# Kernel tuning notes

Hardware: AMD Instinct MI355X
Metric: run time of the kernel (lower is better)

Reference implementation:

```python
import jax, jax.numpy as jnp
import numpy as np

MASK_OUT_VALUE = -10000.0


def setup_inputs() -> dict:
    key = jax.random.key(0)
    k1, k2, k3 = jax.random.split(key, 3)
    B, H, S, D = 2, 16, 2048, 64
    query = jax.random.normal(k1, (B, H, S, D), dtype=jnp.float32)
    key_t = jax.random.normal(k2, (B, H, S, D), dtype=jnp.float32)
    value = jax.random.normal(k3, (B, H, S, D), dtype=jnp.float32)
    # causal mask: (1, 1, S, S), True where attention is allowed
    mask = jnp.tril(jnp.ones((S, S), dtype=bool))[None, None, :, :]
    return {"query": query, "key": key_t, "value": value, "mask": mask}


def reference(query, key, value, mask):
    # scores: (B, H, S, S)
    scale = 1.0 / jnp.sqrt(jnp.asarray(query.shape[-1], query.dtype))
    attn_scores = jnp.einsum("bhqd,bhkd->bhqk", query, key) * scale
    attn_scores = jnp.where(mask, attn_scores,
                            jnp.asarray(MASK_OUT_VALUE, attn_scores.dtype))
    attn_weights = jax.nn.softmax(attn_scores, axis=-1)
    # dropout is identity (p=0 / eval mode)
    attn_output = jnp.einsum("bhqk,bhkd->bhqd", attn_weights, value)
    return attn_output
```

## Files before the change

### kernel.cpp

```cpp
#include <hip/hip_runtime.h>
#include <math.h>


#define S_LEN   2048
#define D_HEAD  64
#define SCALE_L2E 0.18033688011112042f
#define FIXM    8.0f

using bf16x8 = __attribute__((ext_vector_type(8))) short;
using f32x4  = __attribute__((ext_vector_type(4))) float;

__device__ __forceinline__ unsigned int rnd_bf(float f) {
  return __float_as_uint(f) + 0x8000u;
}
__device__ __forceinline__ unsigned short f2bf(float f) {
  return (unsigned short)(rnd_bf(f) >> 16);
}

__device__ __forceinline__ void gl_lds16(const unsigned short* g, unsigned short* l) {
  __builtin_amdgcn_global_load_lds(
      (const __attribute__((address_space(1))) unsigned int*)g,
      (__attribute__((address_space(3))) unsigned int*)l, 16, 0, 0);
}

template <int CTRL>
__device__ __forceinline__ float dppf(float x) {
  return __builtin_bit_cast(float,
      __builtin_amdgcn_update_dpp(0, __builtin_bit_cast(int, x), CTRL, 0xF, 0xF, false));
}
__device__ __forceinline__ float rowsum16(float x) {
  x += dppf<0xB1>(x);
  x += dppf<0x4E>(x);
  x += dppf<0x124>(x);
  x += dppf<0x128>(x);
  return x;
}
__device__ __forceinline__ float rowmax16(float x) {
  x = fmaxf(x, dppf<0xB1>(x));
  x = fmaxf(x, dppf<0x4E>(x));
  x = fmaxf(x, dppf<0x124>(x));
  x = fmaxf(x, dppf<0x128>(x));
  return x;
}

__global__ __launch_bounds__(256, 4)
void prep(const float* __restrict__ Kg, const float* __restrict__ Vg,
          unsigned short* __restrict__ Kb, unsigned short* __restrict__ Vt)
{
  __shared__ __align__(16) unsigned short Lt[64][72];
  const int j = blockIdx.x, t = threadIdx.x;
  const int bh = j >> 4, seg = j & 15;
  const size_t base = (size_t)bh * (S_LEN * D_HEAD) + (size_t)seg * 128 * D_HEAD;
#pragma unroll
  for (int i = 0; i < 8; ++i) {
    const size_t idx = base + i * 1024 + t * 4;
    const f32x4 v = *(const f32x4*)(Kg + idx);
    uint2 pk;
    pk.x = (rnd_bf(v[1]) & 0xFFFF0000u) | (rnd_bf(v[0]) >> 16);
    pk.y = (rnd_bf(v[3]) & 0xFFFF0000u) | (rnd_bf(v[2]) >> 16);
    *(uint2*)(Kb + idx) = pk;
  }
  for (int h = 0; h < 2; ++h) {
    const int s0 = seg * 128 + h * 64;
    __syncthreads();
#pragma unroll
    for (int pp = 0; pp < 4; ++pp) {
      const int r = t >> 2;
      const int d0 = (t & 3) * 4 + pp * 16;
      const f32x4 v = *(const f32x4*)(Vg + (size_t)bh * (S_LEN * D_HEAD)
                                         + (size_t)(s0 + r) * D_HEAD + d0);
#pragma unroll
      for (int e = 0; e < 4; ++e) Lt[d0 + e][r] = f2bf(v[e]);
    }
    __syncthreads();
#pragma unroll
    for (int q = 0; q < 2; ++q) {
      const int d = t >> 2, ch = (t & 3) + 4 * q;
      *(uint4*)(Vt + (size_t)(bh * 64 + d) * S_LEN + s0 + ch * 8) =
          *(const uint4*)&Lt[d][ch * 8];
    }
  }
}

__global__ __launch_bounds__(256, 2)
void fa(const float* __restrict__ Qg, const unsigned short* __restrict__ Kb,
        const unsigned short* __restrict__ Vt, float* __restrict__ Og)
{
  __shared__ unsigned short Ks[2][64][64];
  __shared__ unsigned short Vs[2][64][64];
  __shared__ unsigned short PsLo[4][16][64];
  __shared__ unsigned short PsHi[4][16][64];

  const int id = blockIdx.x;
  const int bh = id & 31;
  const int b  = id >> 5;

  const int t    = threadIdx.x;
  const int w    = t >> 6;
  const int lane = t & 63;
  const int c    = lane & 15;
  const int quad = lane >> 4;

  const float* __restrict__ Qb = Qg + (size_t)bh * (S_LEN * D_HEAD);
  float* __restrict__ Ob = Og + (size_t)bh * (S_LEN * D_HEAD);

  const int lo_row0 = 64 * b + 16 * w;
  const int hi_row0 = S_LEN - 64 * (b + 1) + 16 * w;
  const int ktmax   = 31 - b;

  bf16x8 qlo[2], qhi[2];
  {
    const float* ql = Qb + (size_t)(lo_row0 + c) * D_HEAD + quad * 8;
    const float* qh = Qb + (size_t)(hi_row0 + c) * D_HEAD + quad * 8;
#pragma unroll
    for (int h = 0; h < 2; ++h) {
      f32x4 a0 = *(const f32x4*)(ql + 32 * h);
      f32x4 a1 = *(const f32x4*)(ql + 32 * h + 4);
      f32x4 b0 = *(const f32x4*)(qh + 32 * h);
      f32x4 b1 = *(const f32x4*)(qh + 32 * h + 4);
#pragma unroll
      for (int j = 0; j < 4; ++j) {
        qlo[h][j]     = (short)f2bf(a0[j] * SCALE_L2E);
        qlo[h][4 + j] = (short)f2bf(a1[j] * SCALE_L2E);
        qhi[h][j]     = (short)f2bf(b0[j] * SCALE_L2E);
        qhi[h][4 + j] = (short)f2bf(b1[j] * SCALE_L2E);
      }
    }
  }

  int fOff[4][2];
#pragma unroll
  for (int ci = 0; ci < 4; ++ci)
#pragma unroll
    for (int h = 0; h < 2; ++h)
      fOff[ci][h] = ((ci * 16 + c) << 6) + (((h * 4 + quad) ^ (c & 7)) << 3);
  int pw[4][4];
#pragma unroll
  for (int ci = 0; ci < 4; ++ci)
#pragma unroll
    for (int r = 0; r < 4; ++r) {
      const int prow = quad * 4 + r, pcol = ci * 16 + c;
      pw[ci][r] = (prow << 6) + ((((pcol >> 3) ^ (prow & 7)) << 3) | (pcol & 7));
    }
  int prd[2];
#pragma unroll
  for (int h = 0; h < 2; ++h)
    prd[h] = (c << 6) + (((h * 4 + quad) ^ (c & 7)) << 3);

  f32x4 olo[4], ohi[4];
  float lslo[4], lshi[4];
#pragma unroll
  for (int i = 0; i < 4; ++i) {
    olo[i] = (f32x4){0.f, 0.f, 0.f, 0.f};
    ohi[i] = (f32x4){0.f, 0.f, 0.f, 0.f};
    lslo[i] = 0.f; lshi[i] = 0.f;
  }

  const int rl = lane >> 3;
  const int jj = (lane & 7) ^ rl;
  auto stage = [&](int kt, int buf) {
#pragma unroll
    for (int n = 0; n < 2; ++n) {
      const int row = w * 16 + n * 8 + rl;
      gl_lds16(Kb + (((size_t)(bh * S_LEN + kt * 64 + row)) << 6) + jj * 8,
               &Ks[buf][w * 16 + n * 8][0]);
      gl_lds16(Vt + (((size_t)(bh * 64 + row)) << 11) + kt * 64 + jj * 8,
               &Vs[buf][w * 16 + n * 8][0]);
    }
  };

  auto band = [&](const bf16x8 (&qa)[2], f32x4 (&oacc)[4], float (&ls)[4],
                  unsigned short* psw, const bf16x8 (&kf)[4][2],
                  const bf16x8 (&vf)[4][2], int row0, int kt, bool domask) {
    f32x4 sc[4];
#pragma unroll
    for (int ci = 0; ci < 4; ++ci) {
      f32x4 acc = (f32x4){-FIXM, -FIXM, -FIXM, -FIXM};
      acc = __builtin_amdgcn_mfma_f32_16x16x32_bf16(qa[0], kf[ci][0], acc, 0, 0, 0);
      acc = __builtin_amdgcn_mfma_f32_16x16x32_bf16(qa[1], kf[ci][1], acc, 0, 0, 0);
      sc[ci] = acc;
    }
    if (domask) {
#pragma unroll
      for (int ci = 0; ci < 4; ++ci) {
        const int gcol = kt * 64 + ci * 16 + c;
#pragma unroll
        for (int r = 0; r < 4; ++r)
          if (gcol > row0 + quad * 4 + r) sc[ci][r] = -1e30f;
      }
    }
#pragma unroll
    for (int ci = 0; ci < 4; ++ci)
#pragma unroll
      for (int r = 0; r < 4; ++r)
        sc[ci][r] = __builtin_amdgcn_exp2f(sc[ci][r]);
#pragma unroll
    for (int r = 0; r < 4; ++r)
      ls[r] += (sc[0][r] + sc[1][r]) + (sc[2][r] + sc[3][r]);
#pragma unroll
    for (int ci = 0; ci < 4; ++ci)
#pragma unroll
      for (int r = 0; r < 4; ++r)
        psw[pw[ci][r]] = f2bf(sc[ci][r]);
    const bf16x8 pa0 = *(const bf16x8*)(psw + prd[0]);
    const bf16x8 pa1 = *(const bf16x8*)(psw + prd[1]);
#pragma unroll
    for (int ci = 0; ci < 4; ++ci) {
      oacc[ci] = __builtin_amdgcn_mfma_f32_16x16x32_bf16(pa0, vf[ci][0], oacc[ci], 0, 0, 0);
      oacc[ci] = __builtin_amdgcn_mfma_f32_16x16x32_bf16(pa1, vf[ci][1], oacc[ci], 0, 0, 0);
    }
  };

  stage(0, 0);
  for (int kt = 0; kt <= ktmax; ++kt) {
    const int cur = kt & 1;
    __syncthreads();
    if (kt < ktmax) stage(kt + 1, cur ^ 1);

    const unsigned short* ksc = &Ks[cur][0][0];
    const unsigned short* vsc = &Vs[cur][0][0];
    bf16x8 kf[4][2], vf[4][2];
#pragma unroll
    for (int ci = 0; ci < 4; ++ci)
#pragma unroll
      for (int h = 0; h < 2; ++h) {
        kf[ci][h] = *(const bf16x8*)(ksc + fOff[ci][h]);
        vf[ci][h] = *(const bf16x8*)(vsc + fOff[ci][h]);
      }

    if (kt <= b)
      band(qlo, olo, lslo, &PsLo[w][0][0], kf, vf, lo_row0, kt, kt == b);
    band(qhi, ohi, lshi, &PsHi[w][0][0], kf, vf, hi_row0, kt, kt == ktmax);
  }

  {
    float ilo[4], ihi[4];
#pragma unroll
    for (int r = 0; r < 4; ++r) {
      ilo[r] = 1.0f / rowsum16(lslo[r]);
      ihi[r] = 1.0f / rowsum16(lshi[r]);
    }
#pragma unroll
    for (int ci = 0; ci < 4; ++ci)
#pragma unroll
      for (int r = 0; r < 4; ++r) {
        Ob[(size_t)(lo_row0 + quad * 4 + r) * D_HEAD + ci * 16 + c] = olo[ci][r] * ilo[r];
        Ob[(size_t)(hi_row0 + quad * 4 + r) * D_HEAD + ci * 16 + c] = ohi[ci][r] * ihi[r];
      }
  }
}

__global__ __launch_bounds__(256, 4)
void fa_fb(const float* __restrict__ Qg, const float* __restrict__ Kg,
           const float* __restrict__ Vg, float* __restrict__ Og)
{
  __shared__ __align__(16) unsigned short Ksh[64][72];
  __shared__ __align__(16) unsigned short Vsh[64][72];
  __shared__ __align__(16) unsigned short Psh[4][16][72];
  const int id = blockIdx.x;
  const int bh = id & 31;
  const int p  = id >> 5;
  const int t    = threadIdx.x;
  const int w    = t >> 6;
  const int lane = t & 63;
  const int c    = lane & 15;
  const int quad = lane >> 4;
  const size_t base = (size_t)bh * (S_LEN * D_HEAD);
  const float* __restrict__ Qb = Qg + base;
  const float* __restrict__ Kb = Kg + base;
  const float* __restrict__ Vb = Vg + base;
  float* __restrict__ Ob = Og + base;
  const int wv   = w & 1;
  const int row0 = (w >= 2) ? (S_LEN - 32 * (p + 1) + 16 * wv) : (32 * p + 16 * wv);
  const int ktdiag = row0 >> 6;
  const int ktmax  = (S_LEN - 1 - 32 * p) >> 6;
  bf16x8 qa[2];
  {
    const float* qp = Qb + (size_t)(row0 + c) * D_HEAD + quad * 8;
#pragma unroll
    for (int h = 0; h < 2; ++h) {
      f32x4 a0 = *(const f32x4*)(qp + 32 * h);
      f32x4 a1 = *(const f32x4*)(qp + 32 * h + 4);
#pragma unroll
      for (int j = 0; j < 4; ++j) {
        qa[h][j]     = (short)f2bf(a0[j] * SCALE_L2E);
        qa[h][4 + j] = (short)f2bf(a1[j] * SCALE_L2E);
      }
    }
  }
  f32x4 oa[4];
  float ls[4];
#pragma unroll
  for (int i = 0; i < 4; ++i) {
    oa[i] = (f32x4){0.f, 0.f, 0.f, 0.f};
    ls[i] = 0.f;
  }
  for (int kt = 0; kt <= ktmax; ++kt) {
    __syncthreads();
    {
      const int cp = t & 15;
      const int rg = t >> 4;
      const int col0 = cp * 4;
      const int sw = (cp >> 2) << 3;
#pragma unroll
      for (int i = 0; i < 4; ++i) {
        const int row = i * 16 + rg;
        const size_t goff = (size_t)(kt * 64 + row) * D_HEAD + col0;
        const f32x4 kv = *(const f32x4*)(Kb + goff);
        const f32x4 vv = *(const f32x4*)(Vb + goff);
        const unsigned int k01 = (rnd_bf(kv[1]) & 0xFFFF0000u) | (rnd_bf(kv[0]) >> 16);
        const unsigned int k23 = (rnd_bf(kv[3]) & 0xFFFF0000u) | (rnd_bf(kv[2]) >> 16);
        *(uint2*)&Ksh[row][col0] = make_uint2(k01, k23);
        const int kz = row ^ sw;
#pragma unroll
        for (int e = 0; e < 4; ++e)
          Vsh[col0 + e][kz] = f2bf(vv[e]);
      }
    }
    __syncthreads();
    if (kt <= ktdiag) {
      bf16x8 kf[4][2], vf[4][2];
#pragma unroll
      for (int ci = 0; ci < 4; ++ci) {
        kf[ci][0] = *(const bf16x8*)&Ksh[ci * 16 + c][quad * 8];
        kf[ci][1] = *(const bf16x8*)&Ksh[ci * 16 + c][32 + quad * 8];
        vf[ci][0] = *(const bf16x8*)&Vsh[ci * 16 + c][(quad ^ ci) * 8];
        vf[ci][1] = *(const bf16x8*)&Vsh[ci * 16 + c][32 + ((quad ^ ci) * 8)];
      }
      f32x4 sc[4];
#pragma unroll
      for (int ci = 0; ci < 4; ++ci) {
        f32x4 acc = (f32x4){-FIXM, -FIXM, -FIXM, -FIXM};
        acc = __builtin_amdgcn_mfma_f32_16x16x32_bf16(qa[0], kf[ci][0], acc, 0, 0, 0);
        acc = __builtin_amdgcn_mfma_f32_16x16x32_bf16(qa[1], kf[ci][1], acc, 0, 0, 0);
        sc[ci] = acc;
      }
      if (kt == ktdiag) {
#pragma unroll
        for (int ci = 0; ci < 4; ++ci) {
          const int gcol = kt * 64 + ci * 16 + c;
#pragma unroll
          for (int r = 0; r < 4; ++r)
            if (gcol > row0 + quad * 4 + r) sc[ci][r] = -1e30f;
        }
      }
#pragma unroll
      for (int ci = 0; ci < 4; ++ci)
#pragma unroll
        for (int r = 0; r < 4; ++r)
          sc[ci][r] = __builtin_amdgcn_exp2f(sc[ci][r]);
#pragma unroll
      for (int r = 0; r < 4; ++r)
        ls[r] += (sc[0][r] + sc[1][r]) + (sc[2][r] + sc[3][r]);
#pragma unroll
      for (int ci = 0; ci < 4; ++ci)
#pragma unroll
        for (int r = 0; r < 4; ++r) {
          const int prow = quad * 4 + r;
          Psh[w][prow][(ci * 16 + c) ^ ((prow >> 3) << 3)] = f2bf(sc[ci][r]);
        }
      const int px = (c >> 3) << 3;
      const bf16x8 pa0 = *(const bf16x8*)&Psh[w][c][(quad * 8) ^ px];
      const bf16x8 pa1 = *(const bf16x8*)&Psh[w][c][((32 + quad * 8)) ^ px];
#pragma unroll
      for (int ci = 0; ci < 4; ++ci) {
        oa[ci] = __builtin_amdgcn_mfma_f32_16x16x32_bf16(pa0, vf[ci][0], oa[ci], 0, 0, 0);
        oa[ci] = __builtin_amdgcn_mfma_f32_16x16x32_bf16(pa1, vf[ci][1], oa[ci], 0, 0, 0);
      }
    }
  }
  {
    float inv[4];
#pragma unroll
    for (int r = 0; r < 4; ++r) inv[r] = 1.0f / rowsum16(ls[r]);
#pragma unroll
    for (int ci = 0; ci < 4; ++ci)
#pragma unroll
      for (int r = 0; r < 4; ++r)
        Ob[(size_t)(row0 + quad * 4 + r) * D_HEAD + ci * 16 + c] = oa[ci][r] * inv[r];
  }
}

extern "C" void kernel_launch(void* const* d_in, const int* in_sizes, int n_in,
                              void* d_out, int out_size, void* d_ws, size_t ws_size,
                              hipStream_t stream) {
  (void)in_sizes; (void)n_in; (void)out_size;
  const float* Q = (const float*)d_in[0];
  const float* K = (const float*)d_in[1];
  const float* V = (const float*)d_in[2];
  float* O = (float*)d_out;
  const size_t NEED = 2ull * 32 * S_LEN * D_HEAD * 2;
  if (ws_size >= NEED) {
    unsigned short* Kb = (unsigned short*)d_ws;
    unsigned short* Vt = Kb + (size_t)32 * S_LEN * D_HEAD;
    prep<<<dim3(512), dim3(256), 0, stream>>>(K, V, Kb, Vt);
    fa<<<dim3(512), dim3(256), 0, stream>>>(Q, Kb, Vt, O);
  } else {
    fa_fb<<<dim3(1024), dim3(256), 0, stream>>>(Q, K, V, O);
  }
}
```

Baseline: 142.8 us.

## Split fa work into 1024 blocks, one query band per wave

Each block previously had all four waves process a low and a high 64-row query band together. Now each block covers a 32-row low band (waves 0-1) and a 32-row high band (waves 2-3), and each wave owns a single 16-row band that skips K tiles past its diagonal. The grid doubles to 1024 blocks, launch bounds rise to 4 blocks per CU, and one P staging buffer replaces two. This is meant to raise occupancy and parallelism, at the cost of each K/V tile being staged by twice as many blocks and waves idling on tiles they skip.

```diff
diff --git a/kernel.cpp b/kernel.cpp
--- a/kernel.cpp
+++ b/kernel.cpp
@@ -33,13 +33,6 @@
   x += dppf<0x4E>(x);
   x += dppf<0x124>(x);
   x += dppf<0x128>(x);
-  return x;
-}
-__device__ __forceinline__ float rowmax16(float x) {
-  x = fmaxf(x, dppf<0xB1>(x));
-  x = fmaxf(x, dppf<0x4E>(x));
-  x = fmaxf(x, dppf<0x124>(x));
-  x = fmaxf(x, dppf<0x128>(x));
   return x;
 }
 
@@ -82,18 +75,17 @@
   }
 }
 
-__global__ __launch_bounds__(256, 2)
+__global__ __launch_bounds__(256, 4)
 void fa(const float* __restrict__ Qg, const unsigned short* __restrict__ Kb,
         const unsigned short* __restrict__ Vt, float* __restrict__ Og)
 {
   __shared__ unsigned short Ks[2][64][64];
   __shared__ unsigned short Vs[2][64][64];
-  __shared__ unsigned short PsLo[4][16][64];
-  __shared__ unsigned short PsHi[4][16][64];
+  __shared__ unsigned short Ps[4][16][64];
 
   const int id = blockIdx.x;
   const int bh = id & 31;
-  const int b  = id >> 5;
+  const int p  = id >> 5;
 
   const int t    = threadIdx.x;
   const int w    = t >> 6;
@@ -104,26 +96,23 @@
   const float* __restrict__ Qb = Qg + (size_t)bh * (S_LEN * D_HEAD);
   float* __restrict__ Ob = Og + (size_t)bh * (S_LEN * D_HEAD);
 
-  const int lo_row0 = 64 * b + 16 * w;
-  const int hi_row0 = S_LEN - 64 * (b + 1) + 16 * w;
-  const int ktmax   = 31 - b;
-
-  bf16x8 qlo[2], qhi[2];
+  const int wv   = w & 1;
+  const int row0 = (w >= 2) ? (S_LEN - 32 * (p + 1) + 16 * wv)
+                            : (32 * p + 16 * wv);
+  const int ktdiag = row0 >> 6;
+  const int ktmax  = (S_LEN - 1 - 32 * p) >> 6;
+
+  bf16x8 qa[2];
   {
-    const float* ql = Qb + (size_t)(lo_row0 + c) * D_HEAD + quad * 8;
-    const float* qh = Qb + (size_t)(hi_row0 + c) * D_HEAD + quad * 8;
+    const float* qp = Qb + (size_t)(row0 + c) * D_HEAD + quad * 8;
 #pragma unroll
     for (int h = 0; h < 2; ++h) {
-      f32x4 a0 = *(const f32x4*)(ql + 32 * h);
-      f32x4 a1 = *(const f32x4*)(ql + 32 * h + 4);
-      f32x4 b0 = *(const f32x4*)(qh + 32 * h);
-      f32x4 b1 = *(const f32x4*)(qh + 32 * h + 4);
+      f32x4 a0 = *(const f32x4*)(qp + 32 * h);
+      f32x4 a1 = *(const f32x4*)(qp + 32 * h + 4);
 #pragma unroll
       for (int j = 0; j < 4; ++j) {
-        qlo[h][j]     = (short)f2bf(a0[j] * SCALE_L2E);
-        qlo[h][4 + j] = (short)f2bf(a1[j] * SCALE_L2E);
-        qhi[h][j]     = (short)f2bf(b0[j] * SCALE_L2E);
-        qhi[h][4 + j] = (short)f2bf(b1[j] * SCALE_L2E);
+        qa[h][j]     = (short)f2bf(a0[j] * SCALE_L2E);
+        qa[h][4 + j] = (short)f2bf(a1[j] * SCALE_L2E);
       }
     }
   }
@@ -147,13 +136,12 @@
   for (int h = 0; h < 2; ++h)
     prd[h] = (c << 6) + (((h * 4 + quad) ^ (c & 7)) << 3);
 
-  f32x4 olo[4], ohi[4];
-  float lslo[4], lshi[4];
+  f32x4 oa[4];
+  float ls[4];
 #pragma unroll
   for (int i = 0; i < 4; ++i) {
-    olo[i] = (f32x4){0.f, 0.f, 0.f, 0.f};
-    ohi[i] = (f32x4){0.f, 0.f, 0.f, 0.f};
-    lslo[i] = 0.f; lshi[i] = 0.f;
+    oa[i] = (f32x4){0.f, 0.f, 0.f, 0.f};
+    ls[i] = 0.f;
   }
 
   const int rl = lane >> 3;
@@ -169,84 +157,74 @@
     }
   };
 
-  auto band = [&](const bf16x8 (&qa)[2], f32x4 (&oacc)[4], float (&ls)[4],
-                  unsigned short* psw, const bf16x8 (&kf)[4][2],
-                  const bf16x8 (&vf)[4][2], int row0, int kt, bool domask) {
-    f32x4 sc[4];
-#pragma unroll
-    for (int ci = 0; ci < 4; ++ci) {
-      f32x4 acc = (f32x4){-FIXM, -FIXM, -FIXM, -FIXM};
-      acc = __builtin_amdgcn_mfma_f32_16x16x32_bf16(qa[0], kf[ci][0], acc, 0, 0, 0);
-      acc = __builtin_amdgcn_mfma_f32_16x16x32_bf16(qa[1], kf[ci][1], acc, 0, 0, 0);
-      sc[ci] = acc;
-    }
-    if (domask) {
-#pragma unroll
-      for (int ci = 0; ci < 4; ++ci) {
-        const int gcol = kt * 64 + ci * 16 + c;
-#pragma unroll
-        for (int r = 0; r < 4; ++r)
-          if (gcol > row0 + quad * 4 + r) sc[ci][r] = -1e30f;
-      }
-    }
-#pragma unroll
-    for (int ci = 0; ci < 4; ++ci)
-#pragma unroll
-      for (int r = 0; r < 4; ++r)
-        sc[ci][r] = __builtin_amdgcn_exp2f(sc[ci][r]);
-#pragma unroll
-    for (int r = 0; r < 4; ++r)
-      ls[r] += (sc[0][r] + sc[1][r]) + (sc[2][r] + sc[3][r]);
-#pragma unroll
-    for (int ci = 0; ci < 4; ++ci)
-#pragma unroll
-      for (int r = 0; r < 4; ++r)
-        psw[pw[ci][r]] = f2bf(sc[ci][r]);
-    const bf16x8 pa0 = *(const bf16x8*)(psw + prd[0]);
-    const bf16x8 pa1 = *(const bf16x8*)(psw + prd[1]);
-#pragma unroll
-    for (int ci = 0; ci < 4; ++ci) {
-      oacc[ci] = __builtin_amdgcn_mfma_f32_16x16x32_bf16(pa0, vf[ci][0], oacc[ci], 0, 0, 0);
-      oacc[ci] = __builtin_amdgcn_mfma_f32_16x16x32_bf16(pa1, vf[ci][1], oacc[ci], 0, 0, 0);
-    }
-  };
-
   stage(0, 0);
   for (int kt = 0; kt <= ktmax; ++kt) {
     const int cur = kt & 1;
     __syncthreads();
     if (kt < ktmax) stage(kt + 1, cur ^ 1);
 
-    const unsigned short* ksc = &Ks[cur][0][0];
-    const unsigned short* vsc = &Vs[cur][0][0];
-    bf16x8 kf[4][2], vf[4][2];
+    if (kt <= ktdiag) {
+      const unsigned short* ksc = &Ks[cur][0][0];
+      const unsigned short* vsc = &Vs[cur][0][0];
+      bf16x8 kf[4][2], vf[4][2];
+#pragma unroll
+      for (int ci = 0; ci < 4; ++ci)
+#pragma unroll
+        for (int h = 0; h < 2; ++h) {
+          kf[ci][h] = *(const bf16x8*)(ksc + fOff[ci][h]);
+          vf[ci][h] = *(const bf16x8*)(vsc + fOff[ci][h]);
+        }
+
+      f32x4 sc[4];
+#pragma unroll
+      for (int ci = 0; ci < 4; ++ci) {
+        f32x4 acc = (f32x4){-FIXM, -FIXM, -FIXM, -FIXM};
+        acc = __builtin_amdgcn_mfma_f32_16x16x32_bf16(qa[0], kf[ci][0], acc, 0, 0, 0);
+        acc = __builtin_amdgcn_mfma_f32_16x16x32_bf16(qa[1], kf[ci][1], acc, 0, 0, 0);
+        sc[ci] = acc;
+      }
+      if (kt == ktdiag) {
+#pragma unroll
+        for (int ci = 0; ci < 4; ++ci) {
+          const int gcol = kt * 64 + ci * 16 + c;
+#pragma unroll
+          for (int r = 0; r < 4; ++r)
+            if (gcol > row0 + quad * 4 + r) sc[ci][r] = -1e30f;
+        }
+      }
+#pragma unroll
+      for (int ci = 0; ci < 4; ++ci)
+#pragma unroll
+        for (int r = 0; r < 4; ++r)
+          sc[ci][r] = __builtin_amdgcn_exp2f(sc[ci][r]);
+#pragma unroll
+      for (int r = 0; r < 4; ++r)
+        ls[r] += (sc[0][r] + sc[1][r]) + (sc[2][r] + sc[3][r]);
+      unsigned short* psw = &Ps[w][0][0];
+#pragma unroll
+      for (int ci = 0; ci < 4; ++ci)
+#pragma unroll
+        for (int r = 0; r < 4; ++r)
+          psw[pw[ci][r]] = f2bf(sc[ci][r]);
+      const bf16x8 pa0 = *(const bf16x8*)(psw + prd[0]);
+      const bf16x8 pa1 = *(const bf16x8*)(psw + prd[1]);
+#pragma unroll
+      for (int ci = 0; ci < 4; ++ci) {
+        oa[ci] = __builtin_amdgcn_mfma_f32_16x16x32_bf16(pa0, vf[ci][0], oa[ci], 0, 0, 0);
+        oa[ci] = __builtin_amdgcn_mfma_f32_16x16x32_bf16(pa1, vf[ci][1], oa[ci], 0, 0, 0);
+      }
+    }
+  }
+
+  {
+    float inv[4];
+#pragma unroll
+    for (int r = 0; r < 4; ++r) inv[r] = 1.0f / rowsum16(ls[r]);
 #pragma unroll
     for (int ci = 0; ci < 4; ++ci)
 #pragma unroll
-      for (int h = 0; h < 2; ++h) {
-        kf[ci][h] = *(const bf16x8*)(ksc + fOff[ci][h]);
-        vf[ci][h] = *(const bf16x8*)(vsc + fOff[ci][h]);
-      }
-
-    if (kt <= b)
-      band(qlo, olo, lslo, &PsLo[w][0][0], kf, vf, lo_row0, kt, kt == b);
-    band(qhi, ohi, lshi, &PsHi[w][0][0], kf, vf, hi_row0, kt, kt == ktmax);
-  }
-
-  {
-    float ilo[4], ihi[4];
-#pragma unroll
-    for (int r = 0; r < 4; ++r) {
-      ilo[r] = 1.0f / rowsum16(lslo[r]);
-      ihi[r] = 1.0f / rowsum16(lshi[r]);
-    }
-#pragma unroll
-    for (int ci = 0; ci < 4; ++ci)
-#pragma unroll
-      for (int r = 0; r < 4; ++r) {
-        Ob[(size_t)(lo_row0 + quad * 4 + r) * D_HEAD + ci * 16 + c] = olo[ci][r] * ilo[r];
-        Ob[(size_t)(hi_row0 + quad * 4 + r) * D_HEAD + ci * 16 + c] = ohi[ci][r] * ihi[r];
-      }
+      for (int r = 0; r < 4; ++r)
+        Ob[(size_t)(row0 + quad * 4 + r) * D_HEAD + ci * 16 + c] = oa[ci][r] * inv[r];
   }
 }
 
@@ -394,7 +372,7 @@
     unsigned short* Kb = (unsigned short*)d_ws;
     unsigned short* Vt = Kb + (size_t)32 * S_LEN * D_HEAD;
     prep<<<dim3(512), dim3(256), 0, stream>>>(K, V, Kb, Vt);
-    fa<<<dim3(512), dim3(256), 0, stream>>>(Q, Kb, Vt, O);
+    fa<<<dim3(1024), dim3(256), 0, stream>>>(Q, Kb, Vt, O);
   } else {
     fa_fb<<<dim3(1024), dim3(256), 0, stream>>>(Q, K, V, O);
   }
```

Result: faster. 139.2 us (-2.5%).
